# Kernel optimization log

Hardware: AMD Instinct MI355X
Metric: run time of the kernel (lower is better)

The kernel has to match this reference:

```python
import jax, jax.numpy as jnp
import numpy as np

N = 100000      # total nodes across batched graphs
E = 1600000     # total edges (avg degree 16)
B = 4096        # number of graphs in the batch
DIM_IN = 74
D2 = 200
D3 = 12
H1 = 100        # gc1 output
DG = 20         # gc2 output (d_g)
M1 = 128
M2 = 32
FD = (DG + 1) * (D2 + 1)  # 4221 fusion features
EPS = 1e-5


def _glorot(k, shape):
    lim = float(np.sqrt(6.0 / (shape[0] + shape[1])))
    return jax.random.uniform(k, shape, jnp.float32, -lim, lim)


def setup_inputs() -> dict:
    key = jax.random.key(0)
    ks = jax.random.split(key, 18)
    inp = {
        'feat': jax.random.normal(ks[0], (N, DIM_IN), jnp.float32),
        'desc_2d': jax.random.normal(ks[1], (B, D2), jnp.float32),
        'desc_3d': jax.random.normal(ks[2], (B, D3), jnp.float32),
        'edge_src': jax.random.randint(ks[3], (E,), 0, N, jnp.int32),
        'edge_dst': jax.random.randint(ks[4], (E,), 0, N, jnp.int32),
        'graph_ids': jnp.sort(jax.random.randint(ks[5], (N,), 0, B, jnp.int32)),
        # GCN layer params (Linear inside NodeApplyModule)
        'W_gc1': _glorot(ks[6], (DIM_IN, H1)),
        'b_gc1': jnp.zeros((H1,), jnp.float32),
        'W_gc2': _glorot(ks[7], (H1, DG)),
        'b_gc2': jnp.zeros((DG,), jnp.float32),
        # attention weight W: (d_g, dim_2d_desc)
        'W_attn': _glorot(ks[8], (DG, D2)),
        # MLP
        'W_fc1': _glorot(ks[9], (FD, M1)),
        'b_fc1': jnp.zeros((M1,), jnp.float32),
        'W_fc2': _glorot(ks[10], (M1, M2)),
        'b_fc2': jnp.zeros((M2,), jnp.float32),
        'W_fc3': _glorot(ks[11], (M2, 1)),
        'b_fc3': jnp.zeros((1,), jnp.float32),
        # BatchNorm affine params
        'gamma1': jnp.ones((M1,), jnp.float32),
        'beta1': jnp.zeros((M1,), jnp.float32),
        'gamma2': jnp.ones((M2,), jnp.float32),
        'beta2': jnp.zeros((M2,), jnp.float32),
    }
    return inp


def _mean_agg(h, src, dst):
    # copy_u('h','m') then mean over mailbox; zero in-degree nodes keep h (DGL semantics)
    msg = h[src]                                                   # [E, d] gather
    s = jax.ops.segment_sum(msg, dst, num_segments=N)              # [N, d]
    deg = jax.ops.segment_sum(jnp.ones((src.shape[0],), h.dtype), dst, num_segments=N)
    mean = s / jnp.maximum(deg, 1.0)[:, None]
    return jnp.where((deg > 0)[:, None], mean, h)


def _batchnorm(x, gamma, beta):
    mu = jnp.mean(x, axis=0)
    var = jnp.mean(jnp.square(x - mu), axis=0)  # biased var (training mode)
    return (x - mu) * jax.lax.rsqrt(var + EPS) * gamma + beta


def reference(feat, desc_2d, desc_3d, edge_src, edge_dst, graph_ids,
              W_gc1, b_gc1, W_gc2, b_gc2, W_attn,
              W_fc1, b_fc1, W_fc2, b_fc2, W_fc3, b_fc3,
              gamma1, beta1, gamma2, beta2):
    # GCN layer 1: mean neighbor agg -> linear -> relu
    h = jax.nn.relu(_mean_agg(feat, edge_src, edge_dst) @ W_gc1 + b_gc1)   # [N, 100]
    # GCN layer 2
    h = jax.nn.relu(_mean_agg(h, edge_src, edge_dst) @ W_gc2 + b_gc2)      # [N, 20]
    # dgl.mean_nodes: per-graph mean readout
    sg = jax.ops.segment_sum(h, graph_ids, num_segments=B)                 # [B, 20]
    cnt = jax.ops.segment_sum(jnp.ones((N,), h.dtype), graph_ids, num_segments=B)
    hg = sg / jnp.maximum(cnt, 1.0)[:, None]                               # [B, 20]
    # attention over 2D descriptors
    attn = jax.nn.softmax(hg @ W_attn, axis=-1)                            # [B, 200]
    desc_att = attn * desc_2d
    # augment with ones and take outer product (bmm fusion)
    ones = jnp.ones((hg.shape[0], 1), hg.dtype)
    hg_a = jnp.concatenate([hg, ones], axis=1)                             # [B, 21]
    da_a = jnp.concatenate([desc_att, ones], axis=1)                       # [B, 201]
    fusion = jnp.einsum('bi,bj->bij', hg_a, da_a).reshape(hg.shape[0], -1) # [B, 4221]
    # MLP with BatchNorm (training-mode stats, dropout off)
    out = jax.nn.relu(_batchnorm(fusion @ W_fc1 + b_fc1, gamma1, beta1))
    out = jax.nn.relu(_batchnorm(out @ W_fc2 + b_fc2, gamma2, beta2))
    out = out @ W_fc3 + b_fc3                                              # [B, 1]
    return out
```

## Files before the change

kernel.cpp:

```cpp
#include <hip/hip_runtime.h>

#define NN 100000
#define NE 1600000
#define NB 4096
#define DIN 74
#define DPAD 80
#define DH1 100
#define DGD 20
#define DD2 200
#define DM1 128
#define DM2 32
#define NSEG 8
#define KPAD 4352
#define KSEG 544
#define NBUK 256
#define BNODES 391
#define CAP 7000
#define EPB 3125
#define GOFS_BLKS 64
#define PRE_BUK 512
#define PRE_PREP (KPAD/32 + 2)
typedef unsigned int uint;
typedef unsigned short ushort;
typedef __attribute__((ext_vector_type(8))) short bf16x8;
typedef __attribute__((ext_vector_type(4))) float f32x4;

__device__ __forceinline__ float bf2f(ushort u){ return __uint_as_float(((uint)u)<<16); }
__device__ __forceinline__ ushort f2bf(float f){
  uint u = __float_as_uint(f);
  return (ushort)((u + 0x7fffu + ((u >> 16) & 1u)) >> 16);
}
__device__ __forceinline__ uint bucket_of(int d){
  return (uint)(((unsigned long long)(uint)d * 10984572ull) >> 32);
}
__device__ __forceinline__ void acc2u(float2& a, uint v){
  a.x += __uint_as_float(v << 16);
  a.y += __uint_as_float(v & 0xffff0000u);
}
__device__ __forceinline__ void acc8(float4& a, float4& b, uint4 v){
  a.x += __uint_as_float(v.x << 16);
  a.y += __uint_as_float(v.x & 0xffff0000u);
  a.z += __uint_as_float(v.y << 16);
  a.w += __uint_as_float(v.y & 0xffff0000u);
  b.x += __uint_as_float(v.z << 16);
  b.y += __uint_as_float(v.z & 0xffff0000u);
  b.z += __uint_as_float(v.w << 16);
  b.w += __uint_as_float(v.w & 0xffff0000u);
}

__global__ void k_cvt(const float* __restrict__ feat, ushort* __restrict__ fb){
  int idx = blockIdx.x*256 + threadIdx.x;
  if(idx < NN*DPAD){
    int row = idx / DPAD, d = idx - row*DPAD;
    fb[idx] = (d < DIN) ? f2bf(feat[(size_t)row*DIN + d]) : (ushort)0;
  }
}

__global__ __launch_bounds__(256) void k_pre(
      const int* __restrict__ src, const int* __restrict__ dst,
      int* __restrict__ bukCur, uint2* __restrict__ pairs,
      const float* __restrict__ Wf1, ushort* __restrict__ Bthi,
      const float* __restrict__ W1g, ushort* __restrict__ W1tb,
      const float* __restrict__ W2g, ushort* __restrict__ W2tb){
  __shared__ __align__(16) char SM[35360];
  int blk = blockIdx.x, tid = threadIdx.x;
  if(blk < PRE_BUK){
    uint2* stage = (uint2*)SM;
    ushort* bidx = (ushort*)(SM + 25000);
    int* cnt   = (int*)(SM + 31252);
    int* scanv = (int*)(SM + 32276);
    int* gadj  = (int*)(SM + 33300);
    int* cur   = (int*)(SM + 34324);
    cnt[tid] = 0;
    __syncthreads();
    int e0 = blk * EPB;
    for(int i = tid; i < EPB; i += 256)
      atomicAdd(&cnt[bucket_of(dst[e0 + i])], 1);
    __syncthreads();
    int c = cnt[tid];
    scanv[tid] = c;
    __syncthreads();
    for(int off=1; off<NBUK; off<<=1){
      int v = (tid >= off) ? scanv[tid-off] : 0;
      __syncthreads();
      scanv[tid] += v;
      __syncthreads();
    }
    int excl = scanv[tid] - c;
    int base = atomicAdd(&bukCur[tid], c);
    gadj[tid] = tid*CAP + base - excl;
    cur[tid]  = excl;
    __syncthreads();
    for(int i = tid; i < EPB; i += 256){
      int d = dst[e0 + i];
      int s = src[e0 + i];
      uint b = bucket_of(d);
      int p = atomicAdd(&cur[b], 1);
      stage[p] = make_uint2((uint)s, (uint)d);
      bidx[p] = (ushort)b;
    }
    __syncthreads();
    for(int i = tid; i < EPB; i += 256)
      pairs[(size_t)gadj[bidx[i]] + i] = stage[i];
  } else if(blk < PRE_BUK + KPAD/32){
    float (*Wl)[128] = (float(*)[128])SM;
    int k0 = (blk - PRE_BUK) * 32;
    for(int idx=tid; idx<32*128; idx+=256){
      int kk = idx >> 7, n = idx & 127;
      int k = k0 + kk;
      Wl[kk][n] = (k < 4221) ? Wf1[(size_t)k*128 + n] : 0.f;
    }
    __syncthreads();
    int n = tid >> 1, kh = (tid & 1) * 16;
    uint ph[8];
    #pragma unroll
    for(int e=0;e<8;e++){
      ushort h0 = f2bf(Wl[kh+2*e][n]);
      ushort h1 = f2bf(Wl[kh+2*e+1][n]);
      ph[e] = (uint)h0 | ((uint)h1 << 16);
    }
    uint4* dh = (uint4*)(Bthi + (size_t)n*KPAD + k0 + kh);
    dh[0] = make_uint4(ph[0],ph[1],ph[2],ph[3]);
    dh[1] = make_uint4(ph[4],ph[5],ph[6],ph[7]);
  } else if(blk == PRE_BUK + KPAD/32){
    for(int idx = tid; idx < 112*96; idx += 256){
      int n = idx / 96, k = idx - n*96;
      float v = (n < DH1 && k < DIN) ? W1g[(size_t)k*DH1 + n] : 0.f;
      W1tb[idx] = f2bf(v);
    }
  } else {
    for(int idx = tid; idx < 32*128; idx += 256){
      int n = idx >> 7, k = idx & 127;
      float v = (n < DGD && k < DH1) ? W2g[(size_t)k*DGD + n] : 0.f;
      W2tb[idx] = f2bf(v);
    }
  }
}

__global__ __launch_bounds__(512) void k_csr2(const uint2* __restrict__ pairs,
      const int* __restrict__ bukTot, int* __restrict__ rowptr, int* __restrict__ adj,
      const int* __restrict__ gid, int* __restrict__ gofs){
  if(blockIdx.x >= NBUK){
    int t0 = (blockIdx.x - NBUK)*512 + threadIdx.x;
    for(int i = t0; i <= NN; i += GOFS_BLKS*512){
      int prev = (i == 0) ? -1 : gid[i-1];
      int cur  = (i < NN) ? gid[i] : NB;
      for(int g = prev+1; g <= cur; g++) gofs[g] = i;
    }
    return;
  }
  __shared__ int degL[BNODES];
  __shared__ int curL[BNODES];
  __shared__ int csum[NBUK];
  __shared__ int tsum[512];
  int b = blockIdx.x, tid = threadIdx.x;
  if(tid < NBUK) csum[tid] = bukTot[tid];
  __syncthreads();
  for(int off=1; off<NBUK; off<<=1){
    int v = (tid < NBUK && tid >= off) ? csum[tid-off] : 0;
    __syncthreads();
    if(tid < NBUK) csum[tid] += v;
    __syncthreads();
  }
  int gbase = (b == 0) ? 0 : csum[b-1];
  int tot = bukTot[b];
  int d0 = b*BNODES;
  int nloc = min(BNODES, NN - d0);
  for(int i=tid;i<nloc;i+=512){ degL[i]=0; curL[i]=0; }
  __syncthreads();
  const uint2* pb = pairs + (size_t)b*CAP;
  for(int i=tid;i<tot;i+=512)
    atomicAdd(&degL[(int)pb[i].y - d0], 1);
  __syncthreads();
  int s = (tid < nloc) ? degL[tid] : 0;
  tsum[tid] = s;
  __syncthreads();
  for(int off=1; off<512; off<<=1){
    int v = (tid >= off) ? tsum[tid-off] : 0;
    __syncthreads();
    tsum[tid] += v;
    __syncthreads();
  }
  int excl = tsum[tid] - s;
  if(tid < nloc){
    degL[tid] = excl;
    rowptr[d0 + tid] = gbase + excl;
  }
  if(b == NBUK-1 && tid == 0) rowptr[NN] = gbase + tot;
  __syncthreads();
  for(int i=tid;i<tot;i+=512){
    uint2 pr = pb[i];
    int dl = (int)pr.y - d0;
    int pos = atomicAdd(&curL[dl],1);
    adj[gbase + degL[dl] + pos] = (int)pr.x;
  }
}

__global__ void k_agg1e(const ushort* __restrict__ fb, const float* __restrict__ feat,
                        const int* __restrict__ rowptr, const int* __restrict__ adj,
                        ushort* __restrict__ outb){
  int wid  = (blockIdx.x*blockDim.x + threadIdx.x) >> 6;
  int lane = threadIdx.x & 63;
  if(wid >= NN) return;
  int r0 = rowptr[wid], r1 = rowptr[wid+1];
  int eo = lane / 10;
  int part = lane - eo*10;
  bool act = lane < 60;
  if(!act){ eo = 0; part = 0; }
  float4 la0={0,0,0,0}, ha0={0,0,0,0}, la1={0,0,0,0}, ha1={0,0,0,0};
  float4 la2={0,0,0,0}, ha2={0,0,0,0}, la3={0,0,0,0}, ha3={0,0,0,0};
  for(int j = r0; j < r1; j += 24){
    int j0 = j + eo, j1 = j + 6 + eo, j2 = j + 12 + eo, j3 = j + 18 + eo;
    bool p0 = act && (j0 < r1), p1 = act && (j1 < r1);
    bool p2 = act && (j2 < r1), p3 = act && (j3 < r1);
    int s0 = adj[p0 ? j0 : r0];
    int s1 = adj[p1 ? j1 : r0];
    int s2 = adj[p2 ? j2 : r0];
    int s3 = adj[p3 ? j3 : r0];
    uint4 v0 = *(const uint4*)&fb[(size_t)s0*DPAD + part*8];
    uint4 v1 = *(const uint4*)&fb[(size_t)s1*DPAD + part*8];
    uint4 v2 = *(const uint4*)&fb[(size_t)s2*DPAD + part*8];
    uint4 v3 = *(const uint4*)&fb[(size_t)s3*DPAD + part*8];
    if(p0) acc8(la0, ha0, v0);
    if(p1) acc8(la1, ha1, v1);
    if(p2) acc8(la2, ha2, v2);
    if(p3) acc8(la3, ha3, v3);
  }
  float4 lo, hi;
  lo.x = (la0.x+la1.x)+(la2.x+la3.x); lo.y = (la0.y+la1.y)+(la2.y+la3.y);
  lo.z = (la0.z+la1.z)+(la2.z+la3.z); lo.w = (la0.w+la1.w)+(la2.w+la3.w);
  hi.x = (ha0.x+ha1.x)+(ha2.x+ha3.x); hi.y = (ha0.y+ha1.y)+(ha2.y+ha3.y);
  hi.z = (ha0.z+ha1.z)+(ha2.z+ha3.z); hi.w = (ha0.w+ha1.w)+(ha2.w+ha3.w);
  float4 L1,H1,L2,H2,L3,H3,L4,H4,L5,H5;
  #define SH4(dst,src,off) dst.x=__shfl(src.x,lane+off,64); dst.y=__shfl(src.y,lane+off,64); \
                           dst.z=__shfl(src.z,lane+off,64); dst.w=__shfl(src.w,lane+off,64);
  SH4(L1,lo,10) SH4(H1,hi,10)
  SH4(L2,lo,20) SH4(H2,hi,20)
  SH4(L3,lo,30) SH4(H3,hi,30)
  SH4(L4,lo,40) SH4(H4,hi,40)
  SH4(L5,lo,50) SH4(H5,hi,50)
  #undef SH4
  if(lane < 10){
    float4 tl, th;
    tl.x = ((lo.x+L1.x)+(L2.x+L3.x))+(L4.x+L5.x);
    tl.y = ((lo.y+L1.y)+(L2.y+L3.y))+(L4.y+L5.y);
    tl.z = ((lo.z+L1.z)+(L2.z+L3.z))+(L4.z+L5.z);
    tl.w = ((lo.w+L1.w)+(L2.w+L3.w))+(L4.w+L5.w);
    th.x = ((hi.x+H1.x)+(H2.x+H3.x))+(H4.x+H5.x);
    th.y = ((hi.y+H1.y)+(H2.y+H3.y))+(H4.y+H5.y);
    th.z = ((hi.z+H1.z)+(H2.z+H3.z))+(H4.z+H5.z);
    th.w = ((hi.w+H1.w)+(H2.w+H3.w))+(H4.w+H5.w);
    int d = r1 - r0;
    int dbase = part*8;
    if(d > 0){
      float inv = 1.f/(float)d;
      tl.x*=inv; tl.y*=inv; tl.z*=inv; tl.w*=inv;
      th.x*=inv; th.y*=inv; th.z*=inv; th.w*=inv;
    } else {
      const float* fr = feat + (size_t)wid*DIN;
      tl.x = (dbase+0 < DIN) ? fr[dbase+0] : 0.f;
      tl.y = (dbase+1 < DIN) ? fr[dbase+1] : 0.f;
      tl.z = (dbase+2 < DIN) ? fr[dbase+2] : 0.f;
      tl.w = (dbase+3 < DIN) ? fr[dbase+3] : 0.f;
      th.x = (dbase+4 < DIN) ? fr[dbase+4] : 0.f;
      th.y = (dbase+5 < DIN) ? fr[dbase+5] : 0.f;
      th.z = (dbase+6 < DIN) ? fr[dbase+6] : 0.f;
      th.w = (dbase+7 < DIN) ? fr[dbase+7] : 0.f;
    }
    uint4 o;
    o.x = (uint)f2bf(tl.x) | ((uint)f2bf(tl.y) << 16);
    o.y = (uint)f2bf(tl.z) | ((uint)f2bf(tl.w) << 16);
    o.z = (uint)f2bf(th.x) | ((uint)f2bf(th.y) << 16);
    o.w = (uint)f2bf(th.z) | ((uint)f2bf(th.w) << 16);
    *(uint4*)&outb[(size_t)wid*DPAD + dbase] = o;
  }
}

__global__ __launch_bounds__(256) void k_gcn12(const ushort* __restrict__ Ab80,
      const ushort* __restrict__ W1tb, const ushort* __restrict__ W2tb,
      const float* __restrict__ b1, ushort* __restrict__ y2b){
  __shared__ ushort L[24960];
  ushort* As  = L;
  ushort* Ws  = L + 128*104;
  ushort* Hs  = L;
  ushort* W2s = L + 128*136;
  int tid = threadIdx.x;
  int n0 = blockIdx.x*128;
  #pragma unroll
  for(int p=0;p<5;p++){
    int idx = tid + p*256;
    int row = idx/10, c = (idx - row*10)*8;
    uint4 v = {0,0,0,0};
    if(n0+row < NN) v = *(const uint4*)&Ab80[(size_t)(n0+row)*DPAD + c];
    *(uint4*)&As[row*104 + c] = v;
  }
  { int row = tid>>1, c = 80 + (tid&1)*8;
    *(uint4*)&As[row*104 + c] = (uint4){0,0,0,0}; }
  #pragma unroll
  for(int p=0;p<6;p++){
    int idx = tid + p*256;
    if(idx < 1344){
      int row = idx/12, c = (idx - row*12)*8;
      *(uint4*)&Ws[row*104 + c] = *(const uint4*)&W1tb[row*96 + c];
    }
  }
  __syncthreads();
  int lane = tid & 63, w = tid >> 6;
  int wm = w*32;
  int frow = lane & 15, fk = (lane>>4)*8;
  f32x4 acc[2][7];
  #pragma unroll
  for(int a=0;a<2;a++)
    #pragma unroll
    for(int b=0;b<7;b++) acc[a][b] = (f32x4){0.f,0.f,0.f,0.f};
  #pragma unroll
  for(int ks=0; ks<3; ks++){
    bf16x8 af[2], bfr[7];
    #pragma unroll
    for(int mt=0;mt<2;mt++) af[mt] = *(const bf16x8*)&As[(wm+mt*16+frow)*104 + ks*32 + fk];
    #pragma unroll
    for(int nt=0;nt<7;nt++) bfr[nt] = *(const bf16x8*)&Ws[(nt*16+frow)*104 + ks*32 + fk];
    #pragma unroll
    for(int mt=0;mt<2;mt++)
      #pragma unroll
      for(int nt=0;nt<7;nt++)
        acc[mt][nt] = __builtin_amdgcn_mfma_f32_16x16x32_bf16(af[mt], bfr[nt], acc[mt][nt], 0, 0, 0);
  }
  int crow = (lane>>4)*4, ccol = lane & 15;
  float bv[7];
  #pragma unroll
  for(int nt=0;nt<7;nt++){
    int c = nt*16 + ccol;
    bv[nt] = (c < DH1) ? b1[c] : 0.f;
  }
  __syncthreads();
  #pragma unroll
  for(int mt=0;mt<2;mt++)
    #pragma unroll
    for(int nt=0;nt<7;nt++)
      #pragma unroll
      for(int rr=0;rr<4;rr++)
        Hs[(wm + mt*16 + crow + rr)*136 + nt*16 + ccol] =
            f2bf(fmaxf(acc[mt][nt][rr] + bv[nt], 0.f));
  { int row = tid>>1, c = 112 + (tid&1)*8;
    *(uint4*)&Hs[row*136 + c] = (uint4){0,0,0,0}; }
  #pragma unroll
  for(int p=0;p<2;p++){
    int idx = tid + p*256;
    int row = idx >> 4, c = (idx & 15)*8;
    *(uint4*)&W2s[row*136 + c] = *(const uint4*)&W2tb[row*128 + c];
  }
  __syncthreads();
  f32x4 acc2[2][2];
  #pragma unroll
  for(int a=0;a<2;a++){ acc2[a][0]=(f32x4){0,0,0,0}; acc2[a][1]=(f32x4){0,0,0,0}; }
  #pragma unroll
  for(int ks=0; ks<4; ks++){
    bf16x8 af2[2], bf2r[2];
    #pragma unroll
    for(int mt=0;mt<2;mt++) af2[mt] = *(const bf16x8*)&Hs[(wm+mt*16+frow)*136 + ks*32 + fk];
    #pragma unroll
    for(int nt=0;nt<2;nt++) bf2r[nt] = *(const bf16x8*)&W2s[(nt*16+frow)*136 + ks*32 + fk];
    #pragma unroll
    for(int mt=0;mt<2;mt++)
      #pragma unroll
      for(int nt=0;nt<2;nt++)
        acc2[mt][nt] = __builtin_amdgcn_mfma_f32_16x16x32_bf16(af2[mt], bf2r[nt], acc2[mt][nt], 0, 0, 0);
  }
  #pragma unroll
  for(int mt=0;mt<2;mt++)
    #pragma unroll
    for(int nt=0;nt<2;nt++)
      #pragma unroll
      for(int rr=0;rr<4;rr++){
        int col = nt*16 + ccol;
        int r = n0 + wm + mt*16 + crow + rr;
        if(col < DGD && r < NN)
          y2b[(size_t)r*DGD + col] = f2bf(acc2[mt][nt][rr]);
      }
}

__global__ void k_agg2d(const ushort* __restrict__ y2b, const int* __restrict__ rowptr,
                        const int* __restrict__ adj, const float* __restrict__ b2,
                        float* __restrict__ y3){
  int wid  = (blockIdx.x*blockDim.x + threadIdx.x) >> 6;
  int lane = threadIdx.x & 63;
  if(wid >= NN) return;
  int r0 = rowptr[wid], r1 = rowptr[wid+1];
  int eo = lane / 5;
  int part = lane - eo*5;
  bool act = lane < 60;
  if(!act){ eo = 0; part = 0; }
  float4 a0={0,0,0,0}, a1={0,0,0,0}, a2={0,0,0,0}, a3={0,0,0,0};
  for(int j = r0; j < r1; j += 48){
    int j0 = j + eo, j1 = j + 12 + eo, j2 = j + 24 + eo, j3 = j + 36 + eo;
    bool p0 = act && (j0 < r1), p1 = act && (j1 < r1);
    bool p2 = act && (j2 < r1), p3 = act && (j3 < r1);
    int s0 = adj[p0 ? j0 : r0];
    int s1 = adj[p1 ? j1 : r0];
    int s2 = adj[p2 ? j2 : r0];
    int s3 = adj[p3 ? j3 : r0];
    uint2 v0 = *(const uint2*)&y2b[(size_t)s0*DGD + part*4];
    uint2 v1 = *(const uint2*)&y2b[(size_t)s1*DGD + part*4];
    uint2 v2 = *(const uint2*)&y2b[(size_t)s2*DGD + part*4];
    uint2 v3 = *(const uint2*)&y2b[(size_t)s3*DGD + part*4];
    if(p0){ acc2u(*(float2*)&a0.x, v0.x); acc2u(*(float2*)&a0.z, v0.y); }
    if(p1){ acc2u(*(float2*)&a1.x, v1.x); acc2u(*(float2*)&a1.z, v1.y); }
    if(p2){ acc2u(*(float2*)&a2.x, v2.x); acc2u(*(float2*)&a2.z, v2.y); }
    if(p3){ acc2u(*(float2*)&a3.x, v3.x); acc2u(*(float2*)&a3.z, v3.y); }
  }
  float4 t;
  t.x = (a0.x+a1.x)+(a2.x+a3.x);
  t.y = (a0.y+a1.y)+(a2.y+a3.y);
  t.z = (a0.z+a1.z)+(a2.z+a3.z);
  t.w = (a0.w+a1.w)+(a2.w+a3.w);
  t.x += __shfl(t.x, lane+30, 64); t.y += __shfl(t.y, lane+30, 64);
  t.z += __shfl(t.z, lane+30, 64); t.w += __shfl(t.w, lane+30, 64);
  t.x += __shfl(t.x, lane+15, 64); t.y += __shfl(t.y, lane+15, 64);
  t.z += __shfl(t.z, lane+15, 64); t.w += __shfl(t.w, lane+15, 64);
  float ux = __shfl(t.x, lane+5, 64),  uy = __shfl(t.y, lane+5, 64);
  float uz = __shfl(t.z, lane+5, 64),  uw = __shfl(t.w, lane+5, 64);
  float wx = __shfl(t.x, lane+10, 64), wy = __shfl(t.y, lane+10, 64);
  float wz = __shfl(t.z, lane+10, 64), ww = __shfl(t.w, lane+10, 64);
  if(lane < 5){
    float tx = t.x + ux + wx, ty = t.y + uy + wy;
    float tz = t.z + uz + wz, tw = t.w + uw + ww;
    int d = r1 - r0;
    float bx, by, bz, bw;
    if(d > 0){
      float inv = 1.f/(float)d;
      bx = tx*inv; by = ty*inv; bz = tz*inv; bw = tw*inv;
    } else {
      uint2 v = *(const uint2*)&y2b[(size_t)wid*DGD + lane*4];
      bx = __uint_as_float(v.x << 16);
      by = __uint_as_float(v.x & 0xffff0000u);
      bz = __uint_as_float(v.y << 16);
      bw = __uint_as_float(v.y & 0xffff0000u);
    }
    float4 o;
    o.x = fmaxf(bx + b2[lane*4+0], 0.f);
    o.y = fmaxf(by + b2[lane*4+1], 0.f);
    o.z = fmaxf(bz + b2[lane*4+2], 0.f);
    o.w = fmaxf(bw + b2[lane*4+3], 0.f);
    *(float4*)&y3[(size_t)wid*DGD + lane*4] = o;
  }
}

__global__ __launch_bounds__(256) void k_head3(const float* __restrict__ y3,
      const int* __restrict__ gofs, const float* __restrict__ Wat,
      const float* __restrict__ desc2d, ushort* __restrict__ Ab){
  int g = blockIdx.x, t = threadIdx.x;
  int n0 = gofs[g], n1 = gofs[g+1];
  int cnt = n1 - n0;
  __shared__ float part[240];
  __shared__ float hgaL[21];
  __shared__ float daaL[201];
  __shared__ float red[256];
  if(t < 240){
    int grp = t/20, dim = t - grp*20;
    float a = 0.f;
    for(int n = n0 + grp; n < n1; n += 12) a += y3[(size_t)n*DGD + dim];
    part[t] = a;
  }
  __syncthreads();
  if(t < DGD){
    float s = 0.f;
    #pragma unroll
    for(int k=0;k<12;k++) s += part[k*20 + t];
    hgaL[t] = s / (float)max(cnt, 1);
  }
  if(t == DGD) hgaL[20] = 1.f;
  __syncthreads();
  float logit = 0.f;
  if(t < DD2){
    #pragma unroll
    for(int k=0;k<DGD;k++) logit += hgaL[k]*Wat[k*DD2 + t];
  }
  float v = (t < DD2) ? logit : -1e30f;
  red[t] = v; __syncthreads();
  for(int off=128; off>=1; off>>=1){ if(t<off) red[t]=fmaxf(red[t],red[t+off]); __syncthreads(); }
  float mx = red[0]; __syncthreads();
  float e = (t < DD2) ? expf(logit - mx) : 0.f;
  red[t] = e; __syncthreads();
  for(int off=128; off>=1; off>>=1){ if(t<off) red[t]+=red[t+off]; __syncthreads(); }
  float s = red[0];
  if(t < DD2) daaL[t] = (e/s)*desc2d[(size_t)g*DD2 + t];
  if(t == DD2) daaL[200] = 1.f;
  __syncthreads();
  ushort* arow = Ab + (size_t)g*KPAD;
  #pragma unroll
  for(int p=0;p<17;p++){
    int k = t + 256*p;
    ushort o = 0;
    if(k < 4221){
      int i = (int)(((uint)k * 83470u) >> 24);
      int j = k - i*201;
      o = f2bf(hgaL[i]*daaL[j]);
    }
    arow[k] = o;
  }
}

__global__ __launch_bounds__(256) void k_fuse6(const ushort* __restrict__ Ab,
                                               const ushort* __restrict__ Bthi,
                                               float* __restrict__ zp){
  __shared__ ushort Al[64][40];
  __shared__ ushort Bl[128][40];
  int tid = threadIdx.x;
  int m0 = blockIdx.x * 64;
  int seg = blockIdx.y;
  int lane = tid & 63;
  int w = tid >> 6;
  int wm = (w >> 1) * 32;
  int wn = (w & 1) * 64;
  f32x4 acc[2][4];
  #pragma unroll
  for(int a=0;a<2;a++)
    #pragma unroll
    for(int b=0;b<4;b++) acc[a][b] = (f32x4){0.f,0.f,0.f,0.f};

  int ar = tid >> 2;
  int as = (tid & 3) * 8;
  int br = tid >> 1;
  int bs = (tid & 1) * 16;
  const uint4* gA = (const uint4*)(Ab   + (size_t)(m0 + ar)*KPAD + seg*KSEG + as);
  const uint4* gB = (const uint4*)(Bthi + (size_t)br*KPAD + seg*KSEG + bs);

  int frow = lane & 15;
  int fk   = (lane >> 4) * 8;

  for(int ks=0; ks<17; ks++){
    uint4 va = gA[0];
    uint4 vb0 = gB[0], vb1 = gB[1];
    gA += 4; gB += 4;
    __syncthreads();
    *(uint4*)&Al[ar][as]   = va;
    *(uint4*)&Bl[br][bs]   = vb0;
    *(uint4*)&Bl[br][bs+8] = vb1;
    __syncthreads();
    bf16x8 af[2], bh[4];
    #pragma unroll
    for(int mt=0;mt<2;mt++) af[mt] = *(const bf16x8*)&Al[wm + mt*16 + frow][fk];
    #pragma unroll
    for(int nt=0;nt<4;nt++) bh[nt] = *(const bf16x8*)&Bl[wn + nt*16 + frow][fk];
    #pragma unroll
    for(int mt=0;mt<2;mt++)
      #pragma unroll
      for(int nt=0;nt<4;nt++)
        acc[mt][nt] = __builtin_amdgcn_mfma_f32_16x16x32_bf16(af[mt], bh[nt], acc[mt][nt], 0, 0, 0);
  }
  float* zb = zp + ((size_t)seg*NB + m0)*128;
  int drow = (lane >> 4) * 4;
  int dcol = lane & 15;
  #pragma unroll
  for(int mt=0;mt<2;mt++)
    #pragma unroll
    for(int nt=0;nt<4;nt++)
      #pragma unroll
      for(int rr=0;rr<4;rr++)
        zb[(size_t)(wm + mt*16 + drow + rr)*128 + wn + nt*16 + dcol] = acc[mt][nt][rr];
}

__global__ void k_reduce(const float* __restrict__ zp, const float* __restrict__ b1,
                         float* __restrict__ z1){
  int idx = blockIdx.x*256 + threadIdx.x;
  if(idx >= NB*32) return;
  const float4* z = (const float4*)zp;
  float4 o = ((const float4*)b1)[idx & 31];
  #pragma unroll
  for(int s=0;s<NSEG;s++){
    float4 a = z[idx + (size_t)s*NB*32];
    o.x += a.x; o.y += a.y; o.z += a.z; o.w += a.w;
  }
  ((float4*)z1)[idx] = o;
}

__global__ void k_bnstats(const float* __restrict__ X, int C,
                          const float* __restrict__ gamma, const float* __restrict__ beta,
                          float* __restrict__ scale, float* __restrict__ shift){
  int c = blockIdx.x;
  float s=0.f, s2=0.f;
  for(int r=threadIdx.x; r<NB; r+=256){
    float v = X[(size_t)r*C + c];
    s += v; s2 += v*v;
  }
  __shared__ float sh[256], sh2[256];
  sh[threadIdx.x]=s; sh2[threadIdx.x]=s2;
  __syncthreads();
  for(int off=128; off>=1; off>>=1){
    if(threadIdx.x<off){ sh[threadIdx.x]+=sh[threadIdx.x+off]; sh2[threadIdx.x]+=sh2[threadIdx.x+off]; }
    __syncthreads();
  }
  if(threadIdx.x==0){
    float mu  = sh[0]*(1.0f/NB);
    float var = sh2[0]*(1.0f/NB) - mu*mu;
    float a = gamma[c]*rsqrtf(var + 1e-5f);
    scale[c] = a;
    shift[c] = beta[c] - mu*a;
  }
}

__global__ void k_mlp2(const float* __restrict__ z1, const float* __restrict__ sc,
                       const float* __restrict__ sf, const float* __restrict__ W,
                       const float* __restrict__ bias, float* __restrict__ out){
  __shared__ float Wl[DM1*DM2];
  __shared__ float scl[DM1], sfl[DM1];
  for(int idx=threadIdx.x; idx<DM1*DM2; idx+=256) Wl[idx] = W[idx];
  if(threadIdx.x < DM1){ scl[threadIdx.x]=sc[threadIdx.x]; sfl[threadIdx.x]=sf[threadIdx.x]; }
  __syncthreads();
  int idx = blockIdx.x*256 + threadIdx.x;
  int r = idx >> 5, o = idx & 31;
  if(r >= NB) return;
  float acc = bias[o];
  const float* xr = z1 + (size_t)r*DM1;
  for(int k=0;k<DM1;k++){
    float xn = fmaxf(xr[k]*scl[k] + sfl[k], 0.f);
    acc += xn * Wl[k*DM2 + o];
  }
  out[(size_t)r*DM2 + o] = acc;
}

__global__ void k_final(const float* __restrict__ z2, const float* __restrict__ sc2,
                        const float* __restrict__ sf2, const float* __restrict__ W3,
                        const float* __restrict__ b3, float* __restrict__ out){
  int r = blockIdx.x*256 + threadIdx.x;
  if(r >= NB) return;
  float acc = b3[0];
  const float* xr = z2 + (size_t)r*DM2;
  #pragma unroll
  for(int o=0;o<DM2;o++){
    float xn = fmaxf(xr[o]*sc2[o] + sf2[o], 0.f);
    acc += xn * W3[o];
  }
  out[r] = acc;
}

extern "C" void kernel_launch(void* const* d_in, const int* in_sizes, int n_in,
                              void* d_out, int out_size, void* d_ws, size_t ws_size,
                              hipStream_t stream){
  (void)in_sizes; (void)n_in; (void)out_size; (void)ws_size;
  const float* feat   = (const float*)d_in[0];
  const float* desc2d = (const float*)d_in[1];
  const int*   esrc   = (const int*)d_in[3];
  const int*   edst   = (const int*)d_in[4];
  const int*   gid    = (const int*)d_in[5];
  const float* Wg1    = (const float*)d_in[6];
  const float* bg1    = (const float*)d_in[7];
  const float* Wg2    = (const float*)d_in[8];
  const float* bg2    = (const float*)d_in[9];
  const float* Wat    = (const float*)d_in[10];
  const float* Wf1    = (const float*)d_in[11];
  const float* bf1    = (const float*)d_in[12];
  const float* Wf2    = (const float*)d_in[13];
  const float* bf2    = (const float*)d_in[14];
  const float* Wf3    = (const float*)d_in[15];
  const float* bf3    = (const float*)d_in[16];
  const float* gamma1 = (const float*)d_in[17];
  const float* beta1  = (const float*)d_in[18];
  const float* gamma2 = (const float*)d_in[19];
  const float* beta2  = (const float*)d_in[20];
  float* out = (float*)d_out;

  char* base = (char*)d_ws;
  size_t off = 0;
  auto alloc = [&](size_t bytes)->void*{
    void* r = base + off;
    off = (off + bytes + 255) & ~(size_t)255;
    return r;
  };
  int*    rowptr = (int*)   alloc((size_t)(NN+1)*4);
  int*    gofs   = (int*)   alloc((size_t)(NB+1)*4);
  int*    adj    = (int*)   alloc((size_t)NE*4);
  int*    bukCur = (int*)   alloc((size_t)NBUK*4);
  float*  sc1    = (float*) alloc((size_t)DM1*4);
  float*  sf1    = (float*) alloc((size_t)DM1*4);
  float*  sc2    = (float*) alloc((size_t)DM2*4);
  float*  sf2    = (float*) alloc((size_t)DM2*4);
  ushort* W1thi  = (ushort*)alloc((size_t)128*KPAD*2);
  ushort* W1tb   = (ushort*)alloc((size_t)112*96*2);
  ushort* W2tb   = (ushort*)alloc((size_t)32*128*2);
  float*  z1     = (float*) alloc((size_t)NB*DM1*4);
  float*  z2     = (float*) alloc((size_t)NB*DM2*4);
  char*   R1     = (char*)  alloc((size_t)NN*DPAD*4);
  char*   R2     = (char*)  alloc((size_t)NB*KPAD*2);
  uint2*  pairs  = (uint2*) R1;
  ushort* agg80b = (ushort*)R1;
  float*  zp     = (float*) R1;
  float*  y3     = (float*) (R1 + (size_t)17*1024*1024);
  ushort* featb  = (ushort*)R2;
  ushort* y2b    = (ushort*)(R2 + (size_t)NN*DPAD*2);
  ushort* Ab     = (ushort*)R2;

  hipMemsetAsync(bukCur, 0, (size_t)NBUK*4, stream);

  k_pre <<<PRE_BUK + PRE_PREP, 256, 0, stream>>>(
      esrc, edst, bukCur, pairs, Wf1, W1thi, Wg1, W1tb, Wg2, W2tb);
  k_cvt <<<(NN*DPAD+255)/256, 256, 0, stream>>>(feat, featb);
  k_csr2<<<NBUK + GOFS_BLKS, 512, 0, stream>>>(pairs, bukCur, rowptr, adj, gid, gofs);

  k_agg1e <<<(NN+3)/4, 256, 0, stream>>>(featb, feat, rowptr, adj, agg80b);
  k_gcn12 <<<(NN+127)/128, 256, 0, stream>>>(agg80b, W1tb, W2tb, bg1, y2b);
  k_agg2d <<<(NN+3)/4, 256, 0, stream>>>(y2b, rowptr, adj, bg2, y3);

  k_head3<<<NB, 256, 0, stream>>>(y3, gofs, Wat, desc2d, Ab);
  k_fuse6<<<dim3(64, NSEG), 256, 0, stream>>>(Ab, W1thi, zp);
  k_reduce<<<(NB*32+255)/256, 256, 0, stream>>>(zp, bf1, z1);

  k_bnstats<<<DM1, 256, 0, stream>>>(z1, DM1, gamma1, beta1, sc1, sf1);
  k_mlp2   <<<(NB*DM2)/256, 256, 0, stream>>>(z1, sc1, sf1, Wf2, bf2, z2);
  k_bnstats<<<DM2, 256, 0, stream>>>(z2, DM2, gamma2, beta2, sc2, sf2);
  k_final  <<<(NB+255)/256, 256, 0, stream>>>(z2, sc2, sf2, Wf3, bf3, out);
}
```

Before: 218.0 us.

## Build fusion outer-product tiles on the fly inside the fc1 GEMM

The head kernel no longer writes the full bf16 outer-product matrix [B,4352] to global memory. It writes only the per-graph hg vector (padded to 22) and the bf16 attention-weighted descriptor vector (padded to 204). The GEMM kernel stages these small vectors and a k->(i,j) index table in LDS, then forms each A tile element as a product inside the K loop. This avoids a round trip of about 35 MB through global memory, at the cost of extra LDS reads and multiplies per tile. K segments are halved from 8 to 4, which means fewer partial sums to reduce but only 256 blocks, so there is less parallelism.

```diff
diff --git a/kernel.cpp b/kernel.cpp
--- a/kernel.cpp
+++ b/kernel.cpp
@@ -10,9 +10,9 @@
 #define DD2 200
 #define DM1 128
 #define DM2 32
-#define NSEG 8
+#define NSEG 4
 #define KPAD 4352
-#define KSEG 544
+#define KSEG 1088
 #define NBUK 256
 #define BNODES 391
 #define CAP 7000
@@ -446,15 +446,15 @@
   }
 }
 
-__global__ __launch_bounds__(256) void k_head3(const float* __restrict__ y3,
+__global__ __launch_bounds__(256) void k_head4(const float* __restrict__ y3,
       const int* __restrict__ gofs, const float* __restrict__ Wat,
-      const float* __restrict__ desc2d, ushort* __restrict__ Ab){
+      const float* __restrict__ desc2d, float* __restrict__ hgaF,
+      ushort* __restrict__ daab){
   int g = blockIdx.x, t = threadIdx.x;
   int n0 = gofs[g], n1 = gofs[g+1];
   int cnt = n1 - n0;
   __shared__ float part[240];
   __shared__ float hgaL[21];
-  __shared__ float daaL[201];
   __shared__ float red[256];
   if(t < 240){
     int grp = t/20, dim = t - grp*20;
@@ -484,26 +484,20 @@
   red[t] = e; __syncthreads();
   for(int off=128; off>=1; off>>=1){ if(t<off) red[t]+=red[t+off]; __syncthreads(); }
   float s = red[0];
-  if(t < DD2) daaL[t] = (e/s)*desc2d[(size_t)g*DD2 + t];
-  if(t == DD2) daaL[200] = 1.f;
-  __syncthreads();
-  ushort* arow = Ab + (size_t)g*KPAD;
-  #pragma unroll
-  for(int p=0;p<17;p++){
-    int k = t + 256*p;
-    ushort o = 0;
-    if(k < 4221){
-      int i = (int)(((uint)k * 83470u) >> 24);
-      int j = k - i*201;
-      o = f2bf(hgaL[i]*daaL[j]);
-    }
-    arow[k] = o;
-  }
-}
-
-__global__ __launch_bounds__(256) void k_fuse6(const ushort* __restrict__ Ab,
+  if(t < 21) hgaF[(size_t)g*22 + t] = hgaL[t];
+  if(t == 21) hgaF[(size_t)g*22 + 21] = 0.f;
+  if(t < DD2) daab[(size_t)g*204 + t] = f2bf((e/s)*desc2d[(size_t)g*DD2 + t]);
+  if(t == DD2) daab[(size_t)g*204 + 200] = (ushort)0x3F80;
+  if(t >= 201 && t < 204) daab[(size_t)g*204 + t] = 0;
+}
+
+__global__ __launch_bounds__(256) void k_fuse7(const float* __restrict__ hgaF,
+                                               const ushort* __restrict__ daab,
                                                const ushort* __restrict__ Bthi,
                                                float* __restrict__ zp){
+  __shared__ ushort tab[KSEG];
+  __shared__ float  hga_l[64*22];
+  __shared__ ushort daa_l[64*204];
   __shared__ ushort Al[64][40];
   __shared__ ushort Bl[128][40];
   int tid = threadIdx.x;
@@ -513,28 +507,53 @@
   int w = tid >> 6;
   int wm = (w >> 1) * 32;
   int wn = (w & 1) * 64;
+  for(int idx = tid; idx < 64*22; idx += 256)
+    hga_l[idx] = hgaF[(size_t)m0*22 + idx];
+  {
+    uint* dl = (uint*)daa_l;
+    const uint* ds = (const uint*)(daab + (size_t)m0*204);
+    for(int idx = tid; idx < 64*102; idx += 256) dl[idx] = ds[idx];
+  }
+  for(int kl = tid; kl < KSEG; kl += 256){
+    int k = seg*KSEG + kl;
+    ushort v;
+    if(k < 4221){
+      int i = (int)(((uint)k * 83470u) >> 24);
+      int j = k - i*201;
+      v = (ushort)(i | (j << 5));
+    } else v = 21;
+    tab[kl] = v;
+  }
   f32x4 acc[2][4];
   #pragma unroll
   for(int a=0;a<2;a++)
     #pragma unroll
     for(int b=0;b<4;b++) acc[a][b] = (f32x4){0.f,0.f,0.f,0.f};
 
-  int ar = tid >> 2;
-  int as = (tid & 3) * 8;
+  int arow = tid >> 2;
+  int acol = (tid & 3) * 8;
   int br = tid >> 1;
   int bs = (tid & 1) * 16;
-  const uint4* gA = (const uint4*)(Ab   + (size_t)(m0 + ar)*KPAD + seg*KSEG + as);
   const uint4* gB = (const uint4*)(Bthi + (size_t)br*KPAD + seg*KSEG + bs);
-
   int frow = lane & 15;
   int fk   = (lane >> 4) * 8;
 
-  for(int ks=0; ks<17; ks++){
-    uint4 va = gA[0];
+  for(int ks=0; ks<KSEG/32; ks++){
     uint4 vb0 = gB[0], vb1 = gB[1];
-    gA += 4; gB += 4;
-    __syncthreads();
-    *(uint4*)&Al[ar][as]   = va;
+    gB += 4;
+    __syncthreads();
+    {
+      int klb = ks*32 + acol;
+      uint pk[4];
+      #pragma unroll
+      for(int e=0;e<4;e++){
+        ushort v0 = tab[klb + 2*e], v1 = tab[klb + 2*e + 1];
+        float f0 = hga_l[arow*22 + (v0 & 31)] * bf2f(daa_l[arow*204 + (v0 >> 5)]);
+        float f1 = hga_l[arow*22 + (v1 & 31)] * bf2f(daa_l[arow*204 + (v1 >> 5)]);
+        pk[e] = (uint)f2bf(f0) | ((uint)f2bf(f1) << 16);
+      }
+      *(uint4*)&Al[arow][acol] = make_uint4(pk[0],pk[1],pk[2],pk[3]);
+    }
     *(uint4*)&Bl[br][bs]   = vb0;
     *(uint4*)&Bl[br][bs+8] = vb1;
     __syncthreads();
@@ -679,17 +698,18 @@
   ushort* W1thi  = (ushort*)alloc((size_t)128*KPAD*2);
   ushort* W1tb   = (ushort*)alloc((size_t)112*96*2);
   ushort* W2tb   = (ushort*)alloc((size_t)32*128*2);
+  float*  hgaF   = (float*) alloc((size_t)NB*22*4);
+  ushort* daab   = (ushort*)alloc((size_t)NB*204*2);
   float*  z1     = (float*) alloc((size_t)NB*DM1*4);
   float*  z2     = (float*) alloc((size_t)NB*DM2*4);
   char*   R1     = (char*)  alloc((size_t)NN*DPAD*4);
-  char*   R2     = (char*)  alloc((size_t)NB*KPAD*2);
+  char*   R2     = (char*)  alloc((size_t)NN*DPAD*2 + (size_t)NN*DGD*2);
   uint2*  pairs  = (uint2*) R1;
   ushort* agg80b = (ushort*)R1;
   float*  zp     = (float*) R1;
   float*  y3     = (float*) (R1 + (size_t)17*1024*1024);
   ushort* featb  = (ushort*)R2;
   ushort* y2b    = (ushort*)(R2 + (size_t)NN*DPAD*2);
-  ushort* Ab     = (ushort*)R2;
 
   hipMemsetAsync(bukCur, 0, (size_t)NBUK*4, stream);
 
@@ -702,8 +722,8 @@
   k_gcn12 <<<(NN+127)/128, 256, 0, stream>>>(agg80b, W1tb, W2tb, bg1, y2b);
   k_agg2d <<<(NN+3)/4, 256, 0, stream>>>(y2b, rowptr, adj, bg2, y3);
 
-  k_head3<<<NB, 256, 0, stream>>>(y3, gofs, Wat, desc2d, Ab);
-  k_fuse6<<<dim3(64, NSEG), 256, 0, stream>>>(Ab, W1thi, zp);
+  k_head4<<<NB, 256, 0, stream>>>(y3, gofs, Wat, desc2d, hgaF, daab);
+  k_fuse7<<<dim3(64, NSEG), 256, 0, stream>>>(hgaF, daab, W1thi, zp);
   k_reduce<<<(NB*32+255)/256, 256, 0, stream>>>(zp, bf1, z1);
 
   k_bnstats<<<DM1, 256, 0, stream>>>(z1, DM1, gamma1, beta1, sc1, sf1);
```

Measured after the change: 229.2 us. +5.2%, slower.
